# Optimization experiments

Hardware: AMD Instinct MI355X
Metric: run time of the kernel (lower is better)

The kernel has to match this reference:

```python
import jax, jax.numpy as jnp
import numpy as np

N = 100000   # nodes
E = 1600000  # directed edges (avg degree 16)
IN = 256     # input feature dim


def _gcn_norm(src, dst, n):
    # PyG gcn_norm with unit edge weights: deg computed on destination,
    # norm = deg^{-1/2}[src] * deg^{-1/2}[dst]
    deg = jax.ops.segment_sum(jnp.ones_like(dst, jnp.float32), dst, num_segments=n)
    dinv = jnp.where(deg > 0, jax.lax.rsqrt(deg), 0.0)
    return dinv[src] * dinv[dst]


def _gcn_conv(x, W, b, src, dst, norm, n):
    h = x @ W                          # [N, out] dense transform first (PyG order)
    msg = norm[:, None] * h[src]       # gather + scale  [E+N, out]
    agg = jax.ops.segment_sum(msg, dst, num_segments=n)  # scatter-add
    return agg + b


def setup_inputs() -> dict:
    key = jax.random.key(0)
    ks = jax.random.split(key, 5)
    x = jax.random.normal(ks[0], (N, IN), jnp.float32)
    edge_index = jax.random.randint(ks[1], (2, E), 0, N, dtype=jnp.int32)
    W1 = jax.random.normal(ks[2], (IN, 64), jnp.float32) * (1.0 / np.sqrt(IN))
    b1 = jnp.zeros((64,), jnp.float32)
    W2 = jax.random.normal(ks[3], (64, 32), jnp.float32) * (1.0 / np.sqrt(64))
    b2 = jnp.zeros((32,), jnp.float32)
    Wlin = jax.random.normal(ks[4], (32, 1), jnp.float32) * (1.0 / np.sqrt(32))
    blin = jnp.zeros((1,), jnp.float32)
    return {"x": x, "edge_index": edge_index, "W1": W1, "b1": b1,
            "W2": W2, "b2": b2, "Wlin": Wlin, "blin": blin}


def reference(x, edge_index, W1, b1, W2, b2, Wlin, blin):
    n = x.shape[0]
    loops = jnp.arange(n, dtype=edge_index.dtype)  # add self-loops (GCNConv default)
    src = jnp.concatenate([edge_index[0], loops])
    dst = jnp.concatenate([edge_index[1], loops])
    norm = _gcn_norm(src, dst, n)                  # same for both layers
    h = jax.nn.relu(_gcn_conv(x, W1, b1, src, dst, norm, n))
    h = jax.nn.relu(_gcn_conv(h, W2, b2, src, dst, norm, n))
    return h @ Wlin + blin
```

## Files before the change

### kernel.cpp

```cpp
#include <hip/hip_runtime.h>
#include <hip/hip_fp16.h>
#include <math.h>


#define BSH  9
#define BCAP 12288

typedef _Float16 half8 __attribute__((ext_vector_type(8)));
typedef _Float16 half4 __attribute__((ext_vector_type(4)));
typedef float floatx4 __attribute__((ext_vector_type(4)));

#define XT_STRIDE 40

static __global__ __launch_bounds__(256) void k_wfrag(const float* __restrict__ W1,
                                                      _Float16* __restrict__ w1f,
                                                      int* __restrict__ bkt_cnt) {
    int t = threadIdx.x;
    bkt_cnt[t] = 0;
    for (int idx = t; idx < 2048; idx += 256) {
        int kb = idx >> 8;
        int nt = (idx >> 6) & 3;
        int l  = idx & 63;
        int k0 = kb * 32 + ((l >> 4) << 3);
        int nn = nt * 16 + (l & 15);
        half8 b;
        #pragma unroll
        for (int j = 0; j < 8; ++j) b[j] = (_Float16)W1[(k0 + j) * 64 + nn];
        *(half8*)(w1f + (size_t)idx * 8) = b;
    }
}

static __global__ __launch_bounds__(256) void k_fat(const float* __restrict__ x,
                                                    const _Float16* __restrict__ w1f,
                                                    _Float16* __restrict__ h1f,
                                                    const int* __restrict__ src,
                                                    const int* __restrict__ dst,
                                                    int* __restrict__ bkt_cnt,
                                                    int* __restrict__ epack,
                                                    int n, int e, int nScat) {
    __shared__ alignas(16) char smem[32768 + 128 * XT_STRIDE * 2];
    int t = threadIdx.x;

    if ((int)blockIdx.x < nScat) {
        int*           sp    = (int*)smem;
        unsigned char* sbkt  = (unsigned char*)(smem + 16384);
        int*           cnt   = (int*)(smem + 20480);
        int*           loff  = (int*)(smem + 21504);
        int*           lcur  = (int*)(smem + 22528);
        int*           gbase = (int*)(smem + 23552);
        int*           sh    = (int*)(smem + 24576);
        int cb = blockIdx.x * 4096;
        int cc = min(4096, e - cb);

        cnt[t] = 0;
        __syncthreads();
        int ep[16]; unsigned char eb[16];
        int nv = 0;
        #pragma unroll
        for (int k = 0; k < 16; ++k) {
            int i = cb + k * 256 + t;
            if (i < e) {
                int s = src[i], d = dst[i];
                int b = d >> BSH;
                ep[nv] = ((d & 511) << 17) | s;
                eb[nv] = (unsigned char)b;
                atomicAdd(&cnt[b], 1);
                ++nv;
            }
        }
        __syncthreads();
        int v = cnt[t];
        sh[t] = v;
        __syncthreads();
        for (int o = 1; o < 256; o <<= 1) {
            int u = (t >= o) ? sh[t - o] : 0;
            __syncthreads();
            sh[t] += u;
            __syncthreads();
        }
        loff[t] = sh[t] - v;
        lcur[t] = sh[t] - v;
        if (v > 0) gbase[t] = t * BCAP + atomicAdd(&bkt_cnt[t], v);
        __syncthreads();
        for (int k = 0; k < nv; ++k) {
            int b = eb[k];
            int p = atomicAdd(&lcur[b], 1);
            sp[p] = ep[k];
            sbkt[p] = (unsigned char)b;
        }
        __syncthreads();
        for (int i = t; i < cc; i += 256) {
            int b = sbkt[i];
            epack[gbase[b] + (i - loff[b])] = sp[i];
        }
    } else {
        _Float16* Wl = (_Float16*)smem;
        _Float16* xt = (_Float16*)(smem + 32768);
        {
            const float4* s = (const float4*)w1f;
            float4* d = (float4*)smem;
            #pragma unroll
            for (int i = 0; i < 8; ++i) d[t + i * 256] = s[t + i * 256];
        }

        int l = t & 63;
        int w = t >> 6;
        int r0 = (blockIdx.x - nScat) * 128;
        int kq = (l >> 4) << 3;
        int lrow0 = w * 32 + (l & 15);
        int lrow1 = lrow0 + 16;

        floatx4 acc[2][4];
        #pragma unroll
        for (int mt = 0; mt < 2; ++mt)
            #pragma unroll
            for (int nt = 0; nt < 4; ++nt)
                acc[mt][nt] = (floatx4){0.f, 0.f, 0.f, 0.f};

        #pragma unroll
        for (int kb = 0; kb < 8; ++kb) {
            __syncthreads();
            #pragma unroll
            for (int i = 0; i < 4; ++i) {
                int f   = t + i * 256;
                int row = f >> 3;
                int c4  = f & 7;
                int gr  = r0 + row;
                gr = gr < n ? gr : n - 1;
                float4 v = *(const float4*)(x + (size_t)gr * 256 + kb * 32 + c4 * 4);
                half4 h;
                h[0] = (_Float16)v.x; h[1] = (_Float16)v.y;
                h[2] = (_Float16)v.z; h[3] = (_Float16)v.w;
                *(half4*)(xt + row * XT_STRIDE + c4 * 4) = h;
            }
            __syncthreads();

            half8 a0 = *(const half8*)(xt + lrow0 * XT_STRIDE + kq);
            half8 a1 = *(const half8*)(xt + lrow1 * XT_STRIDE + kq);
            #pragma unroll
            for (int nt = 0; nt < 4; ++nt) {
                half8 b = *(const half8*)(Wl + ((size_t)(kb * 4 + nt) * 64 + l) * 8);
                acc[0][nt] = __builtin_amdgcn_mfma_f32_16x16x32_f16(a0, b, acc[0][nt], 0, 0, 0);
                acc[1][nt] = __builtin_amdgcn_mfma_f32_16x16x32_f16(a1, b, acc[1][nt], 0, 0, 0);
            }
        }

        int quad = l >> 4;
        int col  = l & 15;
        int rb0  = r0 + w * 32;
        #pragma unroll
        for (int mt = 0; mt < 2; ++mt) {
            #pragma unroll
            for (int r = 0; r < 4; ++r) {
                int rr = rb0 + mt * 16 + quad * 4 + r;
                if (rr < n) {
                    _Float16* o = h1f + (size_t)rr * 64 + col;
                    #pragma unroll
                    for (int nt = 0; nt < 4; ++nt)
                        o[nt * 16] = (_Float16)acc[mt][nt][r];
                }
            }
        }
    }
}

static __global__ __launch_bounds__(512) void k_bfinal(const int* __restrict__ bkt_cnt,
                                                       const int* __restrict__ epack,
                                                       float* __restrict__ dinv,
                                                       int* __restrict__ offs,
                                                       int* __restrict__ csr_src, int n) {
    __shared__ int cnt[512], sh[512], lcur[512];
    int t = threadIdx.x;
    int base = blockIdx.x << BSH;
    int e0 = blockIdx.x * BCAP;
    int e1 = e0 + bkt_cnt[blockIdx.x];
    cnt[t] = 0;
    __syncthreads();
    for (int i = e0 + t; i < e1; i += 512) atomicAdd(&cnt[epack[i] >> 17], 1);
    __syncthreads();
    int v = cnt[t];
    if (base + t < n) dinv[base + t] = 1.0f / sqrtf((float)(v + 1));
    sh[t] = v;
    __syncthreads();
    for (int o = 1; o < 512; o <<= 1) {
        int u = (t >= o) ? sh[t - o] : 0;
        __syncthreads();
        sh[t] += u;
        __syncthreads();
    }
    int incl = sh[t];
    if (base + t < n) offs[base + t] = e0 + incl;
    lcur[t] = e0 + incl - v;
    __syncthreads();
    for (int i = e0 + t; i < e1; i += 512) {
        int p = epack[i];
        int d = p >> 17;
        int pos = atomicAdd(&lcur[d], 1);
        csr_src[pos] = p & 0x1FFFF;
    }
}

static __global__ __launch_bounds__(512) void k_wpack(int* __restrict__ csr_src,
                                                      const float* __restrict__ dinv,
                                                      const int* __restrict__ bkt_cnt) {
    int b  = blockIdx.x;
    int e0 = b * BCAP;
    int e1 = e0 + bkt_cnt[b];
    for (int i = e0 + threadIdx.x; i < e1; i += 512) {
        int s = csr_src[i];
        int q = (int)(dinv[s] * 32767.0f + 0.5f);
        csr_src[i] = s | (q << 17);
    }
}

static __global__ __launch_bounds__(256) void k_agg1gemm2(const int* __restrict__ offs,
                                                          const int* __restrict__ csr_src,
                                                          const float* __restrict__ dinv,
                                                          const uint2* __restrict__ h1q,
                                                          const float* __restrict__ b1,
                                                          const float* __restrict__ W2,
                                                          __half2* __restrict__ h2h, int n) {
    __shared__ float Wl[64 * 32];
    __shared__ float aggL[16][64];
    int t = threadIdx.x;
    *(float4*)(Wl + t * 4)        = *(const float4*)(W2 + t * 4);
    *(float4*)(Wl + t * 4 + 1024) = *(const float4*)(W2 + t * 4 + 1024);

    int li = t & 15;
    int ni = t >> 4;
    int node  = blockIdx.x * 16 + ni;
    int nodeC = node < n ? node : n - 1;
    int start = (nodeC & 511) ? offs[nodeC - 1] : (nodeC >> BSH) * BCAP;
    int end   = offs[nodeC];
    float dd  = dinv[nodeC];

    uint2 su = h1q[(size_t)nodeC * 16 + li];
    float2 s01 = __half22float2(*(const __half2*)&su.x);
    float2 s23 = __half22float2(*(const __half2*)&su.y);
    float a0 = dd * s01.x, a1 = dd * s01.y, a2 = dd * s23.x, a3 = dd * s23.y;

    const float QS = 1.0f / 32767.0f;
    int j = start;
    for (; j + 7 < end; j += 8) {
        int pk[8];
        #pragma unroll
        for (int u = 0; u < 8; ++u) pk[u] = csr_src[j + u];
        uint2 vv[8]; float wq[8];
        #pragma unroll
        for (int u = 0; u < 8; ++u) {
            int s = pk[u] & 0x1FFFF;
            wq[u] = (float)(((unsigned)pk[u]) >> 17) * QS;
            vv[u] = h1q[(size_t)s * 16 + li];
        }
        #pragma unroll
        for (int u = 0; u < 8; ++u) {
            float2 v01 = __half22float2(*(const __half2*)&vv[u].x);
            float2 v23 = __half22float2(*(const __half2*)&vv[u].y);
            a0 += wq[u] * v01.x; a1 += wq[u] * v01.y;
            a2 += wq[u] * v23.x; a3 += wq[u] * v23.y;
        }
    }
    for (; j < end; ++j) {
        int p = csr_src[j];
        int s = p & 0x1FFFF;
        float wv = (float)(((unsigned)p) >> 17) * QS;
        uint2 v = h1q[(size_t)s * 16 + li];
        float2 v01 = __half22float2(*(const __half2*)&v.x);
        float2 v23 = __half22float2(*(const __half2*)&v.y);
        a0 += wv * v01.x; a1 += wv * v01.y;
        a2 += wv * v23.x; a3 += wv * v23.y;
    }
    float4 bb = *(const float4*)(b1 + li * 4);
    aggL[ni][li * 4 + 0] = fmaxf(dd * a0 + bb.x, 0.f);
    aggL[ni][li * 4 + 1] = fmaxf(dd * a1 + bb.y, 0.f);
    aggL[ni][li * 4 + 2] = fmaxf(dd * a2 + bb.z, 0.f);
    aggL[ni][li * 4 + 3] = fmaxf(dd * a3 + bb.w, 0.f);
    __syncthreads();

    if (node < n) {
        float s0 = 0.f, s1 = 0.f;
        #pragma unroll
        for (int k = 0; k < 64; ++k) {
            float a = aggL[ni][k];
            float2 wv = *(const float2*)(Wl + k * 32 + li * 2);
            s0 += a * wv.x;
            s1 += a * wv.y;
        }
        h2h[(size_t)node * 16 + li] = __float22half2_rn(make_float2(s0, s1));
    }
}

static __global__ __launch_bounds__(256) void k_gather2f(const int* __restrict__ offs,
                                                         const int* __restrict__ csr_src,
                                                         const float* __restrict__ dinv,
                                                         const uint2* __restrict__ h2q,
                                                         const float* __restrict__ b2,
                                                         const float* __restrict__ Wlin,
                                                         const float* __restrict__ blin,
                                                         float* __restrict__ out, int n) {
    int g    = blockIdx.x * 256 + threadIdx.x;
    int node = g >> 3;
    if (node >= n) return;
    int li = g & 7;
    int start = (node & 511) ? offs[node - 1] : (node >> BSH) * BCAP;
    int end   = offs[node];
    float dd  = dinv[node];

    uint2 su = h2q[(size_t)node * 8 + li];
    float2 s01 = __half22float2(*(const __half2*)&su.x);
    float2 s23 = __half22float2(*(const __half2*)&su.y);
    float a0 = dd * s01.x, a1 = dd * s01.y, a2 = dd * s23.x, a3 = dd * s23.y;

    const float QS = 1.0f / 32767.0f;
    int j = start;
    for (; j + 7 < end; j += 8) {
        int pk[8];
        #pragma unroll
        for (int u = 0; u < 8; ++u) pk[u] = csr_src[j + u];
        uint2 vv[8]; float wq[8];
        #pragma unroll
        for (int u = 0; u < 8; ++u) {
            int s = pk[u] & 0x1FFFF;
            wq[u] = (float)(((unsigned)pk[u]) >> 17) * QS;
            vv[u] = h2q[(size_t)s * 8 + li];
        }
        #pragma unroll
        for (int u = 0; u < 8; ++u) {
            float2 v01 = __half22float2(*(const __half2*)&vv[u].x);
            float2 v23 = __half22float2(*(const __half2*)&vv[u].y);
            a0 += wq[u] * v01.x; a1 += wq[u] * v01.y;
            a2 += wq[u] * v23.x; a3 += wq[u] * v23.y;
        }
    }
    for (; j < end; ++j) {
        int p = csr_src[j];
        int s = p & 0x1FFFF;
        float wv = (float)(((unsigned)p) >> 17) * QS;
        uint2 v = h2q[(size_t)s * 8 + li];
        float2 v01 = __half22float2(*(const __half2*)&v.x);
        float2 v23 = __half22float2(*(const __half2*)&v.y);
        a0 += wv * v01.x; a1 += wv * v01.y;
        a2 += wv * v23.x; a3 += wv * v23.y;
    }
    float4 bb = *(const float4*)(b2 + li * 4);
    float4 wl = *(const float4*)(Wlin + li * 4);
    float val = fmaxf(dd * a0 + bb.x, 0.f) * wl.x +
                fmaxf(dd * a1 + bb.y, 0.f) * wl.y +
                fmaxf(dd * a2 + bb.z, 0.f) * wl.z +
                fmaxf(dd * a3 + bb.w, 0.f) * wl.w;
    val += __shfl_xor(val, 4);
    val += __shfl_xor(val, 2);
    val += __shfl_xor(val, 1);
    if (li == 0) out[node] = val + blin[0];
}

extern "C" void kernel_launch(void* const* d_in, const int* in_sizes, int n_in,
                              void* d_out, int out_size, void* d_ws, size_t ws_size,
                              hipStream_t stream) {
    const float* x    = (const float*)d_in[0];
    const int*   ei   = (const int*)d_in[1];
    const float* W1   = (const float*)d_in[2];
    const float* b1   = (const float*)d_in[3];
    const float* W2   = (const float*)d_in[4];
    const float* b2   = (const float*)d_in[5];
    const float* Wlin = (const float*)d_in[6];
    const float* blin = (const float*)d_in[7];
    float* out = (float*)d_out;

    const int n = in_sizes[0] / 256;
    const int e = in_sizes[1] / 2;
    const int* src = ei;
    const int* dst = ei + e;
    const int nbkt  = (n + (1 << BSH) - 1) >> BSH;
    const int nScat = (e + 4095) / 4096;
    const int nGemm = (n + 127) / 128;

    char* wp = (char*)d_ws;
    _Float16* h1f = (_Float16*)wp;
    uint2*    h1q = (uint2*)wp;       wp += (size_t)n * 32 * 4;
    __half2*  h2h = (__half2*)wp;
    uint2*    h2q = (uint2*)wp;       wp += (size_t)n * 32 * 2;
    float*    dinv = (float*)wp;      wp += (size_t)n * 4;
    int*      offs = (int*)wp;        wp += (size_t)n * 4;
    int*      csr_src = (int*)wp;     wp += (size_t)nbkt * BCAP * 4;
    int*      epack = (int*)wp;       wp += (size_t)nbkt * BCAP * 4;
    int*      bkt_cnt = (int*)wp;     wp += 256 * 4;
    _Float16* w1f = (_Float16*)wp;

    dim3 B(256);
    k_wfrag <<<1, B, 0, stream>>>(W1, w1f, bkt_cnt);
    k_fat   <<<nScat + nGemm, B, 0, stream>>>(x, w1f, h1f, src, dst, bkt_cnt, epack, n, e, nScat);
    k_bfinal<<<nbkt, 512, 0, stream>>>(bkt_cnt, epack, dinv, offs, csr_src, n);
    k_wpack <<<nbkt, 512, 0, stream>>>(csr_src, dinv, bkt_cnt);
    k_agg1gemm2<<<(n + 15) / 16, B, 0, stream>>>(offs, csr_src, dinv, h1q, b1, W2, h2h, n);
    k_gather2f <<<(n * 8 + 255) / 256, B, 0, stream>>>(offs, csr_src, dinv, h2q,
                                                       b2, Wlin, blin, out, n);
}
```

Measured before the change: 290.8 us.

## Load GEMM A fragments straight to registers via wave shuffles, drop LDS staging

Result: no change. 286.9 us (-1.3%).

```diff
diff --git a/kernel.cpp b/kernel.cpp
--- a/kernel.cpp
+++ b/kernel.cpp
@@ -9,8 +9,6 @@
 typedef _Float16 half8 __attribute__((ext_vector_type(8)));
 typedef _Float16 half4 __attribute__((ext_vector_type(4)));
 typedef float floatx4 __attribute__((ext_vector_type(4)));
-
-#define XT_STRIDE 40
 
 static __global__ __launch_bounds__(256) void k_wfrag(const float* __restrict__ W1,
                                                       _Float16* __restrict__ w1f,
@@ -38,7 +36,7 @@
                                                     int* __restrict__ bkt_cnt,
                                                     int* __restrict__ epack,
                                                     int n, int e, int nScat) {
-    __shared__ alignas(16) char smem[32768 + 128 * XT_STRIDE * 2];
+    __shared__ alignas(16) char smem[25600];
     int t = threadIdx.x;
 
     if ((int)blockIdx.x < nScat) {
@@ -94,21 +92,18 @@
             epack[gbase[b] + (i - loff[b])] = sp[i];
         }
     } else {
-        _Float16* Wl = (_Float16*)smem;
-        _Float16* xt = (_Float16*)(smem + 32768);
-        {
-            const float4* s = (const float4*)w1f;
-            float4* d = (float4*)smem;
-            #pragma unroll
-            for (int i = 0; i < 8; ++i) d[t + i * 256] = s[t + i * 256];
-        }
-
         int l = t & 63;
         int w = t >> 6;
         int r0 = (blockIdx.x - nScat) * 128;
-        int kq = (l >> 4) << 3;
-        int lrow0 = w * 32 + (l & 15);
-        int lrow1 = lrow0 + 16;
+
+        const float* sg[2];
+        #pragma unroll
+        for (int mt = 0; mt < 2; ++mt) {
+            int gr = r0 + w * 32 + mt * 16 + (l >> 2);
+            gr = gr < n ? gr : n - 1;
+            sg[mt] = x + (size_t)gr * 256 + (l & 3) * 8;
+        }
+        int sidx = (l & 15) * 4 + (l >> 4);
 
         floatx4 acc[2][4];
         #pragma unroll
@@ -119,29 +114,32 @@
 
         #pragma unroll
         for (int kb = 0; kb < 8; ++kb) {
-            __syncthreads();
-            #pragma unroll
-            for (int i = 0; i < 4; ++i) {
-                int f   = t + i * 256;
-                int row = f >> 3;
-                int c4  = f & 7;
-                int gr  = r0 + row;
-                gr = gr < n ? gr : n - 1;
-                float4 v = *(const float4*)(x + (size_t)gr * 256 + kb * 32 + c4 * 4);
-                half4 h;
-                h[0] = (_Float16)v.x; h[1] = (_Float16)v.y;
-                h[2] = (_Float16)v.z; h[3] = (_Float16)v.w;
-                *(half4*)(xt + row * XT_STRIDE + c4 * 4) = h;
-            }
-            __syncthreads();
-
-            half8 a0 = *(const half8*)(xt + lrow0 * XT_STRIDE + kq);
-            half8 a1 = *(const half8*)(xt + lrow1 * XT_STRIDE + kq);
+            float4 stA[2][2];
+            #pragma unroll
+            for (int mt = 0; mt < 2; ++mt) {
+                stA[mt][0] = *(const float4*)(sg[mt] + kb * 32);
+                stA[mt][1] = *(const float4*)(sg[mt] + kb * 32 + 4);
+            }
+            half8 a[2];
+            #pragma unroll
+            for (int mt = 0; mt < 2; ++mt) {
+                #pragma unroll
+                for (int j = 0; j < 2; ++j) {
+                    float f0 = __shfl(stA[mt][j].x, sidx);
+                    float f1 = __shfl(stA[mt][j].y, sidx);
+                    float f2 = __shfl(stA[mt][j].z, sidx);
+                    float f3 = __shfl(stA[mt][j].w, sidx);
+                    a[mt][j * 4 + 0] = (_Float16)f0;
+                    a[mt][j * 4 + 1] = (_Float16)f1;
+                    a[mt][j * 4 + 2] = (_Float16)f2;
+                    a[mt][j * 4 + 3] = (_Float16)f3;
+                }
+            }
             #pragma unroll
             for (int nt = 0; nt < 4; ++nt) {
-                half8 b = *(const half8*)(Wl + ((size_t)(kb * 4 + nt) * 64 + l) * 8);
-                acc[0][nt] = __builtin_amdgcn_mfma_f32_16x16x32_f16(a0, b, acc[0][nt], 0, 0, 0);
-                acc[1][nt] = __builtin_amdgcn_mfma_f32_16x16x32_f16(a1, b, acc[1][nt], 0, 0, 0);
+                half8 b = *(const half8*)(w1f + ((size_t)(kb * 4 + nt) * 64 + l) * 8);
+                acc[0][nt] = __builtin_amdgcn_mfma_f32_16x16x32_f16(a[0], b, acc[0][nt], 0, 0, 0);
+                acc[1][nt] = __builtin_amdgcn_mfma_f32_16x16x32_f16(a[1], b, acc[1][nt], 0, 0, 0);
             }
         }
 
```
